# Kernel tuning notes

Hardware: AMD Instinct MI355X
Metric: run time of the kernel (lower is better)

## Reference

```python
import jax, jax.numpy as jnp
import numpy as np

N = 10000
E = 320000
D_IN = 256
D_HID = 256
D_OUT = 256


def setup_inputs() -> dict:
    key = jax.random.key(0)
    ks = jax.random.split(key, 6)
    x = jax.random.normal(ks[0], (N, D_IN), dtype=jnp.float32)
    edge_index = jax.random.randint(ks[1], (2, E), 0, N, dtype=jnp.int64)
    s1 = 1.0 / np.sqrt(D_IN)
    s2 = 1.0 / np.sqrt(D_HID)
    W1 = jax.random.uniform(ks[2], (D_IN, D_HID), jnp.float32, -s1, s1)
    b1 = jax.random.uniform(ks[3], (D_HID,), jnp.float32, -s1, s1)
    W2 = jax.random.uniform(ks[4], (D_HID, D_OUT), jnp.float32, -s2, s2)
    b2 = jax.random.uniform(ks[5], (D_OUT,), jnp.float32, -s2, s2)
    return {"x": x, "edge_index": edge_index, "W1": W1, "b1": b1, "W2": W2, "b2": b2}


def reference(x, edge_index, W1, b1, W2, b2):
    # GINConv with default eps=0: h_i = (1+eps)*x_i + sum_{(j->i) in E} x_j
    src = edge_index[0]
    dst = edge_index[1]
    agg = jax.ops.segment_sum(x[src], dst, num_segments=N)  # [N, D_IN]
    h = x + agg  # eps = 0
    # 2-layer MLP: Linear -> ReLU -> Linear
    h = jax.nn.relu(jnp.dot(h, W1) + b1)
    return jnp.dot(h, W2) + b2
```

## Files before the change

### kernel.cpp

```cpp
#include <hip/hip_runtime.h>

#define NN 10000
#define EE 320000
#define DD 256
#define CAP 96
#define POISON 0xAAAAAAAAu

typedef __attribute__((ext_vector_type(8))) short short8;
typedef __attribute__((ext_vector_type(4))) float f32x4;

__device__ __forceinline__ float bf_lo(unsigned u) { return __uint_as_float(u << 16); }
__device__ __forceinline__ float bf_hi(unsigned u) { return __uint_as_float(u & 0xffff0000u); }
__device__ __forceinline__ unsigned short f2bf(float f) {
    unsigned u = __float_as_uint(f);
    u += 0x7fffu + ((u >> 16) & 1u);
    return (unsigned short)(u >> 16);
}

__global__ __launch_bounds__(256) void prep_kernel(
    const float* __restrict__ x, unsigned short* __restrict__ xb,
    const float* __restrict__ W1, const float* __restrict__ W2,
    unsigned short* __restrict__ W1t, unsigned short* __restrict__ W2t,
    const int* __restrict__ src, const int* __restrict__ dst,
    int* __restrict__ counts, unsigned short* __restrict__ slots)
{
    __shared__ float tile[64][65];
    const int bid = blockIdx.x;
    const int tid = threadIdx.x;
    if (bid < 1250) {
        const int i = bid * 2048 + tid * 8;
        const float4 a = *(const float4*)(x + i);
        const float4 b = *(const float4*)(x + i + 4);
        unsigned short o[8] = {f2bf(a.x), f2bf(a.y), f2bf(a.z), f2bf(a.w),
                               f2bf(b.x), f2bf(b.y), f2bf(b.z), f2bf(b.w)};
        *(short8*)(xb + i) = *(short8*)o;
    } else if (bid < 1282) {
        int wid = bid - 1250;
        const float* W = (wid & 16) ? W2 : W1;
        unsigned short* Wt = (wid & 16) ? W2t : W1t;
        wid &= 15;
        const int k0 = (wid & 3) * 64, n0 = (wid >> 2) * 64;
        const int tx = tid & 63, ty = tid >> 6;
        for (int r = ty; r < 64; r += 4)
            tile[r][tx] = W[(size_t)(k0 + r) * 256 + n0 + tx];
        __syncthreads();
        for (int r = ty; r < 64; r += 4)
            Wt[(size_t)(n0 + r) * 256 + k0 + tx] = f2bf(tile[tx][r]);
    } else {
        const int e = (bid - 1282) * 256 + tid;
        const int d = dst[e];
        const int s = src[e];
        const unsigned rank = (unsigned)atomicAdd(&counts[d], 1) - POISON;
        if (rank < CAP) slots[(size_t)d * CAP + rank] = (unsigned short)s;
    }
}

__global__ __launch_bounds__(256) void gather_kernel(
    const unsigned short* __restrict__ xb,
    const int* __restrict__ counts,
    const unsigned short* __restrict__ slots,
    unsigned short* __restrict__ aggb)
{
    const int bid = blockIdx.x;
    const int q = bid / 2500;
    const int node = (bid - q * 2500) * 4 + (threadIdx.x >> 6);
    const int lane = threadIdx.x & 63;
    const int grp = lane >> 3, sub = lane & 7;
    const int qoff = q * 8 + sub;
    const unsigned short* sl = slots + (size_t)node * CAP;
    const uint4* xv = (const uint4*)xb;

    const int craw = counts[node];
    const uint4 self = xv[(size_t)node * 32 + qoff];
    int s0 = (int)sl[grp];
    int s1 = (int)sl[8 + grp];
    int s2 = (int)sl[16 + grp];
    int s3 = (int)sl[24 + grp];
    int s4 = (int)sl[32 + grp];

    int deg = (int)((unsigned)craw - POISON);
    deg = min(max(deg, 0), CAP);

    const bool g0 = (grp      < deg), g1 = (8  + grp < deg), g2 = (16 + grp < deg);
    const bool g3 = (24 + grp < deg), g4 = (32 + grp < deg);
    if (!g0) s0 = node;  if (!g1) s1 = node;  if (!g2) s2 = node;
    if (!g3) s3 = node;  if (!g4) s4 = node;

    uint4 v0 = xv[(size_t)s0 * 32 + qoff];
    uint4 v1 = xv[(size_t)s1 * 32 + qoff];
    uint4 v2 = xv[(size_t)s2 * 32 + qoff];
    uint4 v3 = xv[(size_t)s3 * 32 + qoff];
    uint4 v4 = xv[(size_t)s4 * 32 + qoff];

    float acc[8];
    {
        const unsigned w[4] = {self.x, self.y, self.z, self.w};
#pragma unroll
        for (int t = 0; t < 4; ++t) {
            acc[2 * t]     = grp ? 0.f : bf_lo(w[t]);
            acc[2 * t + 1] = grp ? 0.f : bf_hi(w[t]);
        }
    }

#define ZMASK(v, g) if (!(g)) { (v).x = 0; (v).y = 0; (v).z = 0; (v).w = 0; }
#define ACC4(v) { \
        acc[0] += bf_lo((v).x); acc[1] += bf_hi((v).x); \
        acc[2] += bf_lo((v).y); acc[3] += bf_hi((v).y); \
        acc[4] += bf_lo((v).z); acc[5] += bf_hi((v).z); \
        acc[6] += bf_lo((v).w); acc[7] += bf_hi((v).w); }

    ZMASK(v0, g0); ACC4(v0);
    ZMASK(v1, g1); ACC4(v1);
    ZMASK(v2, g2); ACC4(v2);
    ZMASK(v3, g3); ACC4(v3);
    ZMASK(v4, g4); ACC4(v4);

    int j = 40;
    for (; j + 8 <= deg; j += 8) {
        const int s = (int)sl[j + grp];
        uint4 v = xv[(size_t)s * 32 + qoff];
        ACC4(v);
    }
    if (j < deg) {
        const int k = j + grp;
        const bool valid = k < deg;
        const int s = valid ? (int)sl[k] : node;
        uint4 v = xv[(size_t)s * 32 + qoff];
        ZMASK(v, valid);
        ACC4(v);
    }
#undef ACC4
#undef ZMASK

#pragma unroll
    for (int m = 8; m <= 32; m <<= 1)
#pragma unroll
        for (int t = 0; t < 8; ++t)
            acc[t] += __shfl_xor(acc[t], m, 64);

    if (grp == 0) {
        unsigned o[4];
#pragma unroll
        for (int t = 0; t < 4; ++t)
            o[t] = (unsigned)f2bf(acc[2 * t]) | ((unsigned)f2bf(acc[2 * t + 1]) << 16);
        ((uint4*)aggb)[(size_t)node * 32 + qoff] = make_uint4(o[0], o[1], o[2], o[3]);
    }
}

__global__ __launch_bounds__(256) void mlp_kernel(
    const unsigned short* __restrict__ aggb,
    const unsigned short* __restrict__ W1t,
    const unsigned short* __restrict__ W2t,
    const float* __restrict__ b1,
    const float* __restrict__ b2,
    float* __restrict__ out, int M)
{
    __shared__ unsigned short h1[48][264];
    const int tid = threadIdx.x;
    const int wv = tid >> 6, lane = tid & 63;
    const int quad = lane >> 4, l16 = lane & 15;
    const int m0 = blockIdx.x * 48;
    const int n0 = wv * 64;

    int rows[3];
#pragma unroll
    for (int mi = 0; mi < 3; ++mi) {
        int r = m0 + mi * 16 + l16;
        rows[mi] = r < M ? r : M - 1;
    }
    const short* Ap  = (const short*)aggb;
    const short* W1p = (const short*)W1t;
    const short* W2p = (const short*)W2t;

    f32x4 acc[3][4] = {};
#pragma unroll
    for (int kk = 0; kk < 256; kk += 32) {
        const int ko = kk + quad * 8;
        short8 a[3];
#pragma unroll
        for (int mi = 0; mi < 3; ++mi)
            a[mi] = *(const short8*)(Ap + (size_t)rows[mi] * 256 + ko);
#pragma unroll
        for (int j = 0; j < 4; ++j) {
            const short8 b = *(const short8*)(W1p + (size_t)(n0 + j * 16 + l16) * 256 + ko);
#pragma unroll
            for (int mi = 0; mi < 3; ++mi)
                acc[mi][j] = __builtin_amdgcn_mfma_f32_16x16x32_bf16(a[mi], b, acc[mi][j], 0, 0, 0);
        }
    }
#pragma unroll
    for (int j = 0; j < 4; ++j) {
        const int col = n0 + j * 16 + l16;
        const float bs = b1[col];
#pragma unroll
        for (int mi = 0; mi < 3; ++mi)
#pragma unroll
            for (int r = 0; r < 4; ++r) {
                const int row = mi * 16 + quad * 4 + r;
                h1[row][col] = f2bf(fmaxf(acc[mi][j][r] + bs, 0.f));
            }
    }
    __syncthreads();

    f32x4 acc2[3][4] = {};
#pragma unroll
    for (int kk = 0; kk < 256; kk += 32) {
        const int ko = kk + quad * 8;
        short8 a[3];
#pragma unroll
        for (int mi = 0; mi < 3; ++mi)
            a[mi] = *(const short8*)&h1[mi * 16 + l16][ko];
#pragma unroll
        for (int j = 0; j < 4; ++j) {
            const short8 b = *(const short8*)(W2p + (size_t)(n0 + j * 16 + l16) * 256 + ko);
#pragma unroll
            for (int mi = 0; mi < 3; ++mi)
                acc2[mi][j] = __builtin_amdgcn_mfma_f32_16x16x32_bf16(a[mi], b, acc2[mi][j], 0, 0, 0);
        }
    }
#pragma unroll
    for (int j = 0; j < 4; ++j) {
        const int col = n0 + j * 16 + l16;
        const float bs = b2[col];
#pragma unroll
        for (int mi = 0; mi < 3; ++mi)
#pragma unroll
            for (int r = 0; r < 4; ++r) {
                const int row = m0 + mi * 16 + quad * 4 + r;
                if (row < M)
                    out[(size_t)row * 256 + col] = acc2[mi][j][r] + bs;
            }
    }
}

extern "C" void kernel_launch(void* const* d_in, const int* in_sizes, int n_in,
                              void* d_out, int out_size, void* d_ws, size_t ws_size,
                              hipStream_t stream)
{
    const float* x   = (const float*)d_in[0];
    const int*   ei  = (const int*)d_in[1];
    const float* W1  = (const float*)d_in[2];
    const float* b1  = (const float*)d_in[3];
    const float* W2  = (const float*)d_in[4];
    const float* b2  = (const float*)d_in[5];
    float* out = (float*)d_out;

    const int E = in_sizes[1] / 2;
    const int* src = ei;
    const int* dst = ei + E;

    unsigned short* xb   = (unsigned short*)d_ws;
    unsigned short* aggb = xb + (size_t)NN * DD;
    unsigned short* W1t  = aggb + (size_t)NN * DD;
    unsigned short* W2t  = W1t + 256 * 256;
    int* counts = (int*)(W2t + 256 * 256);
    unsigned short* slots = (unsigned short*)(counts + NN);

    prep_kernel<<<2532, 256, 0, stream>>>(x, xb, W1, W2, W1t, W2t,
                                          src, dst, counts, slots);
    gather_kernel<<<NN, 256, 0, stream>>>(xb, counts, slots, aggb);
    mlp_kernel<<<(NN + 47) / 48, 256, 0, stream>>>(aggb, W1t, W2t, b1, b2, out, NN);

    (void)E; (void)ws_size; (void)n_in; (void)out_size;
}
```

Baseline: 130.0 us.

## Fuse prep, gather and MLP into one cooperative persistent kernel

Replaces the three launches (prep, gather, MLP) with a single cooperative kernel whose grid is sized from occupancy. The phases are separated by grid.sync and loop over virtual blocks, which removes launch gaps and tail effects between the kernels. The old three-kernel path stays as a fallback if the cooperative launch fails. The costs are grid-wide barrier overhead, a fixed grid size that may underfill the MLP phase (only 209 tiles), and the occupancy query on the host.

Result: slower. 384.2 us (+195.5%).

```diff
diff --git a/kernel.cpp b/kernel.cpp
--- a/kernel.cpp
+++ b/kernel.cpp
@@ -1,4 +1,7 @@
 #include <hip/hip_runtime.h>
+#include <hip/hip_cooperative_groups.h>
+
+namespace cg = cooperative_groups;
 
 #define NN 10000
 #define EE 320000
@@ -15,6 +18,230 @@
     unsigned u = __float_as_uint(f);
     u += 0x7fffu + ((u >> 16) & 1u);
     return (unsigned short)(u >> 16);
+}
+
+__global__ __launch_bounds__(256, 4) void mega_kernel(
+    const float* __restrict__ x,
+    const int* __restrict__ src, const int* __restrict__ dst,
+    const float* __restrict__ W1, const float* __restrict__ W2,
+    const float* __restrict__ b1, const float* __restrict__ b2,
+    float* __restrict__ out,
+    unsigned short* __restrict__ xb, unsigned short* __restrict__ aggb,
+    unsigned short* __restrict__ W1t, unsigned short* __restrict__ W2t,
+    int* __restrict__ counts, unsigned short* __restrict__ slots)
+{
+    __shared__ union {
+        float tile[64][65];
+        unsigned short h1[48][264];
+    } sm;
+    const int tid = threadIdx.x;
+    const int GRID = (int)gridDim.x;
+    cg::grid_group grid = cg::this_grid();
+
+    for (int vb = blockIdx.x; vb < 2532; vb += GRID) {
+        if (vb < 1250) {
+            const int i = vb * 2048 + tid * 8;
+            const float4 a = *(const float4*)(x + i);
+            const float4 b = *(const float4*)(x + i + 4);
+            unsigned short o[8] = {f2bf(a.x), f2bf(a.y), f2bf(a.z), f2bf(a.w),
+                                   f2bf(b.x), f2bf(b.y), f2bf(b.z), f2bf(b.w)};
+            *(short8*)(xb + i) = *(short8*)o;
+        } else if (vb < 1282) {
+            int wid = vb - 1250;
+            const float* W = (wid & 16) ? W2 : W1;
+            unsigned short* Wt = (wid & 16) ? W2t : W1t;
+            wid &= 15;
+            const int k0 = (wid & 3) * 64, n0 = (wid >> 2) * 64;
+            const int tx = tid & 63, ty = tid >> 6;
+            for (int r = ty; r < 64; r += 4)
+                sm.tile[r][tx] = W[(size_t)(k0 + r) * 256 + n0 + tx];
+            __syncthreads();
+            for (int r = ty; r < 64; r += 4)
+                Wt[(size_t)(n0 + r) * 256 + k0 + tx] = f2bf(sm.tile[tx][r]);
+            __syncthreads();
+        } else {
+            const int e = (vb - 1282) * 256 + tid;
+            const int d = dst[e];
+            const int s = src[e];
+            const unsigned rank = (unsigned)atomicAdd(&counts[d], 1) - POISON;
+            if (rank < CAP) slots[(size_t)d * CAP + rank] = (unsigned short)s;
+        }
+    }
+    __threadfence();
+    grid.sync();
+
+    {
+        const int lane = tid & 63;
+        const int wave = tid >> 6;
+        const int grp = lane >> 3, sub = lane & 7;
+        const uint4* xv = (const uint4*)xb;
+
+        for (int vb = blockIdx.x; vb < 10000; vb += GRID) {
+            const int q = vb / 2500;
+            const int node = (vb - q * 2500) * 4 + wave;
+            const int qoff = q * 8 + sub;
+            const unsigned short* sl = slots + (size_t)node * CAP;
+
+            const int craw = counts[node];
+            const uint4 self = xv[(size_t)node * 32 + qoff];
+            int s0 = (int)sl[grp];
+            int s1 = (int)sl[8 + grp];
+            int s2 = (int)sl[16 + grp];
+            int s3 = (int)sl[24 + grp];
+            int s4 = (int)sl[32 + grp];
+
+            int deg = (int)((unsigned)craw - POISON);
+            deg = min(max(deg, 0), CAP);
+
+            const bool g0 = (grp      < deg), g1 = (8  + grp < deg), g2 = (16 + grp < deg);
+            const bool g3 = (24 + grp < deg), g4 = (32 + grp < deg);
+            if (!g0) s0 = node;  if (!g1) s1 = node;  if (!g2) s2 = node;
+            if (!g3) s3 = node;  if (!g4) s4 = node;
+
+            uint4 v0 = xv[(size_t)s0 * 32 + qoff];
+            uint4 v1 = xv[(size_t)s1 * 32 + qoff];
+            uint4 v2 = xv[(size_t)s2 * 32 + qoff];
+            uint4 v3 = xv[(size_t)s3 * 32 + qoff];
+            uint4 v4 = xv[(size_t)s4 * 32 + qoff];
+
+            float acc[8];
+            {
+                const unsigned w[4] = {self.x, self.y, self.z, self.w};
+#pragma unroll
+                for (int t = 0; t < 4; ++t) {
+                    acc[2 * t]     = grp ? 0.f : bf_lo(w[t]);
+                    acc[2 * t + 1] = grp ? 0.f : bf_hi(w[t]);
+                }
+            }
+
+#define ZMASK(v, g) if (!(g)) { (v).x = 0; (v).y = 0; (v).z = 0; (v).w = 0; }
+#define ACC4(v) { \
+            acc[0] += bf_lo((v).x); acc[1] += bf_hi((v).x); \
+            acc[2] += bf_lo((v).y); acc[3] += bf_hi((v).y); \
+            acc[4] += bf_lo((v).z); acc[5] += bf_hi((v).z); \
+            acc[6] += bf_lo((v).w); acc[7] += bf_hi((v).w); }
+
+            ZMASK(v0, g0); ACC4(v0);
+            ZMASK(v1, g1); ACC4(v1);
+            ZMASK(v2, g2); ACC4(v2);
+            ZMASK(v3, g3); ACC4(v3);
+            ZMASK(v4, g4); ACC4(v4);
+
+            int j = 40;
+            for (; j + 8 <= deg; j += 8) {
+                const int s = (int)sl[j + grp];
+                uint4 v = xv[(size_t)s * 32 + qoff];
+                ACC4(v);
+            }
+            if (j < deg) {
+                const int k = j + grp;
+                const bool valid = k < deg;
+                const int s = valid ? (int)sl[k] : node;
+                uint4 v = xv[(size_t)s * 32 + qoff];
+                ZMASK(v, valid);
+                ACC4(v);
+            }
+#undef ACC4
+#undef ZMASK
+
+#pragma unroll
+            for (int m = 8; m <= 32; m <<= 1)
+#pragma unroll
+                for (int t = 0; t < 8; ++t)
+                    acc[t] += __shfl_xor(acc[t], m, 64);
+
+            if (grp == 0) {
+                unsigned o[4];
+#pragma unroll
+                for (int t = 0; t < 4; ++t)
+                    o[t] = (unsigned)f2bf(acc[2 * t]) | ((unsigned)f2bf(acc[2 * t + 1]) << 16);
+                ((uint4*)aggb)[(size_t)node * 32 + qoff] = make_uint4(o[0], o[1], o[2], o[3]);
+            }
+        }
+    }
+    __threadfence();
+    grid.sync();
+
+    {
+        const int wv = tid >> 6, lane = tid & 63;
+        const int quad = lane >> 4, l16 = lane & 15;
+        const int n0 = wv * 64;
+        const short* Ap  = (const short*)aggb;
+        const short* W1p = (const short*)W1t;
+        const short* W2p = (const short*)W2t;
+        const int M = NN;
+
+        for (int vb = blockIdx.x; vb < 209; vb += GRID) {
+            const int m0 = vb * 48;
+            int rows[3];
+#pragma unroll
+            for (int mi = 0; mi < 3; ++mi) {
+                int r = m0 + mi * 16 + l16;
+                rows[mi] = r < M ? r : M - 1;
+            }
+
+            f32x4 acc[3][4] = {};
+#pragma unroll
+            for (int kk = 0; kk < 256; kk += 32) {
+                const int ko = kk + quad * 8;
+                short8 a[3];
+#pragma unroll
+                for (int mi = 0; mi < 3; ++mi)
+                    a[mi] = *(const short8*)(Ap + (size_t)rows[mi] * 256 + ko);
+#pragma unroll
+                for (int j = 0; j < 4; ++j) {
+                    const short8 b = *(const short8*)(W1p + (size_t)(n0 + j * 16 + l16) * 256 + ko);
+#pragma unroll
+                    for (int mi = 0; mi < 3; ++mi)
+                        acc[mi][j] = __builtin_amdgcn_mfma_f32_16x16x32_bf16(a[mi], b, acc[mi][j], 0, 0, 0);
+                }
+            }
+#pragma unroll
+            for (int j = 0; j < 4; ++j) {
+                const int col = n0 + j * 16 + l16;
+                const float bs = b1[col];
+#pragma unroll
+                for (int mi = 0; mi < 3; ++mi)
+#pragma unroll
+                    for (int r = 0; r < 4; ++r) {
+                        const int row = mi * 16 + quad * 4 + r;
+                        sm.h1[row][col] = f2bf(fmaxf(acc[mi][j][r] + bs, 0.f));
+                    }
+            }
+            __syncthreads();
+
+            f32x4 acc2[3][4] = {};
+#pragma unroll
+            for (int kk = 0; kk < 256; kk += 32) {
+                const int ko = kk + quad * 8;
+                short8 a[3];
+#pragma unroll
+                for (int mi = 0; mi < 3; ++mi)
+                    a[mi] = *(const short8*)&sm.h1[mi * 16 + l16][ko];
+#pragma unroll
+                for (int j = 0; j < 4; ++j) {
+                    const short8 b = *(const short8*)(W2p + (size_t)(n0 + j * 16 + l16) * 256 + ko);
+#pragma unroll
+                    for (int mi = 0; mi < 3; ++mi)
+                        acc2[mi][j] = __builtin_amdgcn_mfma_f32_16x16x32_bf16(a[mi], b, acc2[mi][j], 0, 0, 0);
+                }
+            }
+#pragma unroll
+            for (int j = 0; j < 4; ++j) {
+                const int col = n0 + j * 16 + l16;
+                const float bs = b2[col];
+#pragma unroll
+                for (int mi = 0; mi < 3; ++mi)
+#pragma unroll
+                    for (int r = 0; r < 4; ++r) {
+                        const int row = m0 + mi * 16 + quad * 4 + r;
+                        if (row < M)
+                            out[(size_t)row * 256 + col] = acc2[mi][j][r] + bs;
+                    }
+            }
+            __syncthreads();
+        }
+    }
 }
 
 __global__ __launch_bounds__(256) void prep_kernel(
@@ -256,10 +483,31 @@
     int* counts = (int*)(W2t + 256 * 256);
     unsigned short* slots = (unsigned short*)(counts + NN);
 
-    prep_kernel<<<2532, 256, 0, stream>>>(x, xb, W1, W2, W1t, W2t,
-                                          src, dst, counts, slots);
-    gather_kernel<<<NN, 256, 0, stream>>>(xb, counts, slots, aggb);
-    mlp_kernel<<<(NN + 47) / 48, 256, 0, stream>>>(aggb, W1t, W2t, b1, b2, out, NN);
+    int nb = 0;
+    hipError_t qerr = hipOccupancyMaxActiveBlocksPerMultiprocessor(
+        &nb, (const void*)mega_kernel, 256, 0);
+
+    bool coop_ok = false;
+    if (qerr == hipSuccess && nb > 0) {
+        int grid = nb * 256;
+        if (grid > 2048) grid = 2048;
+        void* args[] = {
+            (void*)&x, (void*)&src, (void*)&dst, (void*)&W1, (void*)&W2,
+            (void*)&b1, (void*)&b2, (void*)&out, (void*)&xb, (void*)&aggb,
+            (void*)&W1t, (void*)&W2t, (void*)&counts, (void*)&slots
+        };
+        hipError_t lerr = hipLaunchCooperativeKernel((void*)mega_kernel,
+                                                     dim3(grid), dim3(256),
+                                                     args, 0, stream);
+        coop_ok = (lerr == hipSuccess);
+    }
+
+    if (!coop_ok) {
+        prep_kernel<<<2532, 256, 0, stream>>>(x, xb, W1, W2, W1t, W2t,
+                                              src, dst, counts, slots);
+        gather_kernel<<<NN, 256, 0, stream>>>(xb, counts, slots, aggb);
+        mlp_kernel<<<(NN + 47) / 48, 256, 0, stream>>>(aggb, W1t, W2t, b1, b2, out, NN);
+    }
 
     (void)E; (void)ws_size; (void)n_in; (void)out_size;
 }
```
